# Kernel optimization log

Hardware: AMD Instinct MI355X
Metric: run time of the kernel (lower is better)

The kernel has to match this reference:

```python
import jax, jax.numpy as jnp
import numpy as np

B, S, E = 2, 2048, 1024
H, D = 16, 64


def setup_inputs() -> dict:
    key = jax.random.key(0)
    ks = jax.random.split(key, 9)
    s_in = 1.0 / np.sqrt(E)
    s_out = 1.0 / np.sqrt(H * D)
    return {
        "x": jax.random.normal(ks[0], (B, S, E), dtype=jnp.float32),
        "W_q": jax.random.uniform(ks[1], (H, E, D), jnp.float32, -s_in, s_in),
        "b_q": jax.random.uniform(ks[2], (H, D), jnp.float32, -s_in, s_in),
        "W_k": jax.random.uniform(ks[3], (H, E, D), jnp.float32, -s_in, s_in),
        "b_k": jax.random.uniform(ks[4], (H, D), jnp.float32, -s_in, s_in),
        "W_v": jax.random.uniform(ks[5], (H, E, D), jnp.float32, -s_in, s_in),
        "b_v": jax.random.uniform(ks[6], (H, D), jnp.float32, -s_in, s_in),
        "W_o": jax.random.uniform(ks[7], (H * D, E), jnp.float32, -s_out, s_out),
        "b_o": jax.random.uniform(ks[8], (E,), jnp.float32, -s_out, s_out),
    }


def reference(x, W_q, b_q, W_k, b_k, W_v, b_v, W_o, b_o):
    # batched per-head projections: [B,S,E] x [H,E,D] -> [B,H,S,D]
    q = jnp.einsum("bse,hed->bhsd", x, W_q) + b_q[None, :, None, :]
    k = jnp.einsum("bse,hed->bhsd", x, W_k) + b_k[None, :, None, :]
    v = jnp.einsum("bse,hed->bhsd", x, W_v) + b_v[None, :, None, :]
    scale = 1.0 / jnp.sqrt(jnp.asarray(D, dtype=x.dtype))
    score = jnp.einsum("bhsd,bhtd->bhst", q, k) * scale  # [B,H,S,S]
    causal = jnp.tril(jnp.ones((S, S), dtype=bool))
    score = jnp.where(causal[None, None], score, -jnp.inf)
    w = jax.nn.softmax(score, axis=-1)
    o = jnp.einsum("bhst,bhtd->bhsd", w, v)  # [B,H,S,D]
    # concat heads along last dim (head-major order matches torch.cat)
    o = o.transpose(0, 2, 1, 3).reshape(B, S, H * D)
    # dropout is identity in eval mode
    return o @ W_o + b_o
```

## Files before the change

kernel.cpp:

```cpp
#include <hip/hip_runtime.h>


typedef __attribute__((ext_vector_type(8)))  __bf16 bf16x8;
typedef __attribute__((ext_vector_type(4)))  __bf16 bf16x4;
typedef __attribute__((ext_vector_type(2)))  __bf16 bf16x2;
typedef __attribute__((ext_vector_type(4)))  float  f32x4;
typedef __attribute__((ext_vector_type(16))) float  f32x16;
typedef __attribute__((ext_vector_type(2)))  unsigned int u32x2;
typedef __attribute__((ext_vector_type(4)))  unsigned int u32x4;

#define LOG2E 1.4426950408889634f
#define SM_SC (0.125f * LOG2E)

static __device__ __forceinline__ void gl2lds16(const void* g, void* l) {
    __builtin_amdgcn_global_load_lds(
        (__attribute__((address_space(1))) void*)(void*)g,
        (__attribute__((address_space(3))) void*)l, 16, 0, 0);
}

static __device__ __forceinline__ unsigned pku(float a, float b) {
    bf16x2 t = { (__bf16)a, (__bf16)b };
    return __builtin_bit_cast(unsigned, t);
}

__global__ void prep_x_kern(const float* __restrict__ x, __bf16* __restrict__ xb) {
    int i = (blockIdx.x * 256 + threadIdx.x) * 4;
    f32x4 v = *(const f32x4*)(x + i);
    bf16x4 o = { (__bf16)v[0], (__bf16)v[1], (__bf16)v[2], (__bf16)v[3] };
    *(bf16x4*)(xb + i) = o;
}

__global__ void __launch_bounds__(256)
prep_wqkv_kern(const float* __restrict__ Wq, const float* __restrict__ Wk,
               const float* __restrict__ Wv, const float* __restrict__ bq,
               const float* __restrict__ bk, const float* __restrict__ bv,
               __bf16* __restrict__ wt, float* __restrict__ bias) {
    __shared__ float T[64][65];
    const int t = threadIdx.x;
    const int blk = blockIdx.x;
    const int kt = blk & 15, ph = blk >> 4;
    const int h = ph & 15, p = ph >> 4;
    const float* W  = (p == 0) ? Wq : (p == 1) ? Wk : Wv;
    const float* bb = (p == 0) ? bq : (p == 1) ? bk : bv;
    #pragma unroll
    for (int i = 0; i < 4; ++i) {
        int flat = i * 1024 + t * 4;
        int kr = flat >> 6, d4 = flat & 63;
        f32x4 v = *(const f32x4*)(W + (h << 16) + ((kt * 64 + kr) << 6) + d4);
        T[kr][d4] = v[0]; T[kr][d4 + 1] = v[1]; T[kr][d4 + 2] = v[2]; T[kr][d4 + 3] = v[3];
    }
    __syncthreads();
    const int d = t >> 2, kq = (t & 3) << 4;
    bf16x8 o0, o1;
    #pragma unroll
    for (int j = 0; j < 8; ++j) o0[j] = (__bf16)T[kq + j][d];
    #pragma unroll
    for (int j = 0; j < 8; ++j) o1[j] = (__bf16)T[kq + 8 + j][d];
    __bf16* dst = wt + (((size_t)(p * 1024 + h * 64 + d)) << 10) + kt * 64 + kq;
    *(bf16x8*)dst = o0;
    *(bf16x8*)(dst + 8) = o1;
    if (kt == 0 && t < 64) bias[p * 1024 + h * 64 + t] = bb[h * 64 + t];
}

__global__ void __launch_bounds__(256)
prep_wo_kern(const float* __restrict__ Wo, __bf16* __restrict__ wt) {
    __shared__ float T[64][65];
    const int t = threadIdx.x;
    const int nt = blockIdx.x & 15, ktile = blockIdx.x >> 4;
    #pragma unroll
    for (int i = 0; i < 4; ++i) {
        int flat = i * 1024 + t * 4;
        int kr = flat >> 6, n4 = flat & 63;
        f32x4 v = *(const f32x4*)(Wo + ((size_t)(ktile * 64 + kr) << 10) + nt * 64 + n4);
        T[kr][n4] = v[0]; T[kr][n4 + 1] = v[1]; T[kr][n4 + 2] = v[2]; T[kr][n4 + 3] = v[3];
    }
    __syncthreads();
    const int n = t >> 2, kq = (t & 3) << 4;
    bf16x8 o0, o1;
    #pragma unroll
    for (int j = 0; j < 8; ++j) o0[j] = (__bf16)T[kq + j][n];
    #pragma unroll
    for (int j = 0; j < 8; ++j) o1[j] = (__bf16)T[kq + 8 + j][n];
    __bf16* dst = wt + (((size_t)(nt * 64 + n)) << 10) + ktile * 64 + kq;
    *(bf16x8*)dst = o0;
    *(bf16x8*)(dst + 8) = o1;
}

template <int EPI>
__global__ void __launch_bounds__(256, 2)
gemm_bt(const __bf16* __restrict__ A, const __bf16* __restrict__ Bt,
        const float* __restrict__ bias,
        __bf16* __restrict__ outq, __bf16* __restrict__ outk, __bf16* __restrict__ outv,
        float* __restrict__ outf)
{
    __shared__ __align__(16) __bf16 As[128 * 64];
    __shared__ __align__(16) __bf16 Bs[128 * 64];
    const int tid = threadIdx.x;
    const int wid = tid >> 6, lane = tid & 63;
    const int r = lane & 15, g = lane >> 4;
    const int m0 = blockIdx.y << 7, n0 = blockIdx.x << 7;
    const int wr = wid >> 1, wc = wid & 1;
    f32x4 acc[4][4] = {};
    for (int k0 = 0; k0 < 1024; k0 += 64) {
        #pragma unroll
        for (int c = 0; c < 4; ++c) {
            int cq = (c * 4 + wid) * 64 + lane;
            int row = cq >> 3, ci = cq & 7;
            gl2lds16(A  + (((size_t)(m0 + row)) << 10) + k0 + ci * 8, As + (c * 4 + wid) * 512);
            gl2lds16(Bt + (((size_t)(n0 + row)) << 10) + k0 + ci * 8, Bs + (c * 4 + wid) * 512);
        }
        __syncthreads();
        bf16x8 af[2][4], bfr[2][4];
        #pragma unroll
        for (int kh = 0; kh < 2; ++kh)
            #pragma unroll
            for (int i = 0; i < 4; ++i) {
                af[kh][i]  = *(const bf16x8*)&As[(wr * 64 + i * 16 + r) * 64 + kh * 32 + g * 8];
                bfr[kh][i] = *(const bf16x8*)&Bs[(wc * 64 + i * 16 + r) * 64 + kh * 32 + g * 8];
            }
        #pragma unroll
        for (int kh = 0; kh < 2; ++kh)
            #pragma unroll
            for (int mi = 0; mi < 4; ++mi)
                #pragma unroll
                for (int ni = 0; ni < 4; ++ni)
                    acc[mi][ni] = __builtin_amdgcn_mfma_f32_16x16x32_bf16(
                        af[kh][mi], bfr[kh][ni], acc[mi][ni], 0, 0, 0);
        __syncthreads();
    }
    if (EPI == 0) {
        #pragma unroll
        for (int ni = 0; ni < 4; ++ni) {
            int n = n0 + wc * 64 + ni * 16 + r;
            float bv = bias[n];
            int p = n >> 10, rem = n & 1023, h = rem >> 6, d = rem & 63;
            #pragma unroll
            for (int mi = 0; mi < 4; ++mi) {
                int mb = m0 + wr * 64 + mi * 16 + g * 4;
                int b = mb >> 11, s = mb & 2047;
                f32x4 v = acc[mi][ni];
                if (p < 2) {
                    __bf16* dst = (p == 0) ? outq : outk;
                    size_t base = (((size_t)(b * 16 + h)) * 2048 + s) * 64 + d;
                    #pragma unroll
                    for (int j = 0; j < 4; ++j)
                        dst[base + (size_t)j * 64] = (__bf16)(v[j] + bv);
                } else {
                    bf16x4 pk = { (__bf16)(v[0] + bv), (__bf16)(v[1] + bv),
                                  (__bf16)(v[2] + bv), (__bf16)(v[3] + bv) };
                    *(bf16x4*)&outv[(((size_t)(b * 16 + h)) * 64 + d) * 2048 + s] = pk;
                }
            }
        }
    } else {
        #pragma unroll
        for (int ni = 0; ni < 4; ++ni) {
            int n = n0 + wc * 64 + ni * 16 + r;
            float bv = bias[n];
            #pragma unroll
            for (int mi = 0; mi < 4; ++mi) {
                int mb = m0 + wr * 64 + mi * 16 + g * 4;
                f32x4 v = acc[mi][ni];
                #pragma unroll
                for (int j = 0; j < 4; ++j)
                    outf[((size_t)(mb + j) << 10) + n] = v[j] + bv;
            }
        }
    }
}

__global__ void __launch_bounds__(256, 3)
attn_kern(const __bf16* __restrict__ q, const __bf16* __restrict__ k,
          const __bf16* __restrict__ vT, __bf16* __restrict__ pO0,
          __bf16* __restrict__ pO1, float* __restrict__ ml)
{
    __shared__ __align__(16) __bf16 Ks [2][64][72];
    __shared__ __align__(16) __bf16 VsT[2][64][72];
    const int tid = threadIdx.x, lane = tid & 63, w = tid >> 6;
    const int r31 = lane & 31, hi = lane >> 5;
    const int x = blockIdx.x & 7, kvh = blockIdx.x >> 3;
    const int bh = blockIdx.y, b = bh >> 4, h = bh & 15;
    const __bf16* qh  = q  + ((size_t)bh << 17);
    const __bf16* khp = k  + ((size_t)bh << 17);
    const __bf16* vhp = vT + ((size_t)bh << 17);
    __bf16* pO = kvh ? pO1 : pO0;
    const int srow = tid >> 3, sci = tid & 7;

    bf16x8 onesf;
    #pragma unroll
    for (int j = 0; j < 8; ++j) onesf[j] = (__bf16)1.0f;

    for (int seg = 0; seg < 2; ++seg) {
        const int xq = (seg == 0) ? (15 - x) : x;
        const int qb0 = xq << 7;
        const int wrow0 = qb0 + w * 32;
        const int mg = wrow0 + r31;
        const int tbeg = kvh * (xq + 1), tend = tbeg + (xq + 1);

        bf16x8 qf[4];
        #pragma unroll
        for (int kk = 0; kk < 4; ++kk)
            qf[kk] = *(const bf16x8*)&qh[(size_t)mg * 64 + kk * 16 + hi * 8];

        f32x16 oacc[2] = {};
        f32x16 lacc = {};
        float mrun = -3.0e38f;

        #pragma unroll
        for (int it = 0; it < 2; ++it) {
            int row = srow + it * 32;
            *(bf16x8*)&Ks [0][row][sci * 8] = *(const bf16x8*)&khp[(size_t)(tbeg * 64 + row) * 64 + sci * 8];
            *(bf16x8*)&VsT[0][row][sci * 8] = *(const bf16x8*)&vhp[(size_t)row * 2048 + tbeg * 64 + sci * 8];
        }
        __syncthreads();

        for (int t = tbeg; t < tend; ++t) {
            const int cur = (t - tbeg) & 1, nxt = cur ^ 1;
            const int n0 = t << 6;
            const bool pre = (t + 1 < tend);
            bf16x8 nk[2], nv[2];
            if (pre) {
                int n1 = n0 + 64;
                #pragma unroll
                for (int it = 0; it < 2; ++it) {
                    int row = srow + it * 32;
                    nk[it] = *(const bf16x8*)&khp[(size_t)(n1 + row) * 64 + sci * 8];
                    nv[it] = *(const bf16x8*)&vhp[(size_t)row * 2048 + n1 + sci * 8];
                }
            }
            if (n0 <= wrow0 + 31) {
                f32x16 sacc[2] = {};
                #pragma unroll
                for (int kk = 0; kk < 4; ++kk) {
                    bf16x8 kf0 = *(const bf16x8*)&Ks[cur][r31]     [kk * 16 + hi * 8];
                    bf16x8 kf1 = *(const bf16x8*)&Ks[cur][32 + r31][kk * 16 + hi * 8];
                    sacc[0] = __builtin_amdgcn_mfma_f32_32x32x16_bf16(kf0, qf[kk], sacc[0], 0, 0, 0);
                    sacc[1] = __builtin_amdgcn_mfma_f32_32x32x16_bf16(kf1, qf[kk], sacc[1], 0, 0, 0);
                }
                if (n0 + 63 > wrow0) {
                    #pragma unroll
                    for (int nf = 0; nf < 2; ++nf)
                        #pragma unroll
                        for (int i = 0; i < 16; ++i) {
                            int n = n0 + nf * 32 + (i & 3) + 8 * (i >> 2) + 4 * hi;
                            if (n > mg) sacc[nf][i] = -3.0e38f;
                        }
                }
                float mx[16];
                #pragma unroll
                for (int i = 0; i < 16; ++i) mx[i] = fmaxf(sacc[0][i], sacc[1][i]);
                #pragma unroll
                for (int s = 8; s > 0; s >>= 1)
                    #pragma unroll
                    for (int i = 0; i < 8; ++i)
                        if (i < s) mx[i] = fmaxf(mx[i], mx[i + s]);
                float pmh = mx[0];
                if (!__all((pmh - mrun) * SM_SC <= 8.0f)) {
                    float pm = fmaxf(pmh, __shfl_xor(pmh, 32));
                    float mnew = fmaxf(mrun, pm);
                    float fac = exp2f((mrun - mnew) * SM_SC);
                    lacc[0] *= fac;
                    #pragma unroll
                    for (int df = 0; df < 2; ++df)
                        #pragma unroll
                        for (int i = 0; i < 16; ++i) oacc[df][i] *= fac;
                    mrun = mnew;
                }
                #pragma unroll
                for (int nf = 0; nf < 2; ++nf)
                    #pragma unroll
                    for (int i = 0; i < 16; ++i)
                        sacc[nf][i] = exp2f((sacc[nf][i] - mrun) * SM_SC);
                #pragma unroll
                for (int nf = 0; nf < 2; ++nf) {
                    unsigned pk[8];
                    #pragma unroll
                    for (int j = 0; j < 8; ++j)
                        pk[j] = pku(sacc[nf][2 * j], sacc[nf][2 * j + 1]);
#if __has_builtin(__builtin_amdgcn_permlane32_swap)
                    u32x2 s02 = __builtin_amdgcn_permlane32_swap(pk[0], pk[2], false, false);
                    u32x2 s13 = __builtin_amdgcn_permlane32_swap(pk[1], pk[3], false, false);
                    u32x2 s46 = __builtin_amdgcn_permlane32_swap(pk[4], pk[6], false, false);
                    u32x2 s57 = __builtin_amdgcn_permlane32_swap(pk[5], pk[7], false, false);
                    u32x4 fw0 = { s02[0], s13[0], s02[1], s13[1] };
                    u32x4 fw1 = { s46[0], s57[0], s46[1], s57[1] };
#else
                    unsigned rxa = __shfl_xor(hi ? pk[0] : pk[2], 32);
                    unsigned rxb = __shfl_xor(hi ? pk[1] : pk[3], 32);
                    unsigned rxc = __shfl_xor(hi ? pk[4] : pk[6], 32);
                    unsigned rxd = __shfl_xor(hi ? pk[5] : pk[7], 32);
                    u32x4 fw0 = { hi ? rxa : pk[0], hi ? rxb : pk[1],
                                  hi ? pk[2] : rxa, hi ? pk[3] : rxb };
                    u32x4 fw1 = { hi ? rxc : pk[4], hi ? rxd : pk[5],
                                  hi ? pk[6] : rxc, hi ? pk[7] : rxd };
#endif
                    bf16x8 pf0 = __builtin_bit_cast(bf16x8, fw0);
                    bf16x8 pf1 = __builtin_bit_cast(bf16x8, fw1);
                    #pragma unroll
                    for (int kl = 0; kl < 2; ++kl) {
                        const bf16x8 pf = kl ? pf1 : pf0;
                        const int kk = nf * 2 + kl;
                        bf16x8 af0 = *(const bf16x8*)&VsT[cur][r31]     [kk * 16 + hi * 8];
                        bf16x8 af1 = *(const bf16x8*)&VsT[cur][32 + r31][kk * 16 + hi * 8];
                        oacc[0] = __builtin_amdgcn_mfma_f32_32x32x16_bf16(af0, pf, oacc[0], 0, 0, 0);
                        oacc[1] = __builtin_amdgcn_mfma_f32_32x32x16_bf16(af1, pf, oacc[1], 0, 0, 0);
                        lacc    = __builtin_amdgcn_mfma_f32_32x32x16_bf16(onesf, pf, lacc, 0, 0, 0);
                    }
                }
            }
            if (pre) {
                #pragma unroll
                for (int it = 0; it < 2; ++it) {
                    int row = srow + it * 32;
                    *(bf16x8*)&Ks [nxt][row][sci * 8] = nk[it];
                    *(bf16x8*)&VsT[nxt][row][sci * 8] = nv[it];
                }
            }
            __syncthreads();
        }
        float lrun = lacc[0];
        float inv = (lrun > 0.f) ? 1.0f / lrun : 0.f;
        #pragma unroll
        for (int df = 0; df < 2; ++df)
            #pragma unroll
            for (int td = 0; td < 8; ++td) {
                bf16x2 pr = { (__bf16)(oacc[df][2 * td] * inv),
                              (__bf16)(oacc[df][2 * td + 1] * inv) };
                int d = df * 32 + 8 * (td >> 1) + 4 * hi + 2 * (td & 1);
                *(bf16x2*)&pO[((size_t)(b * 2048 + mg) << 10) + h * 64 + d] = pr;
            }
        if (hi == 0) {
            size_t mi = (((size_t)kvh * 32 + bh) * 2048 + mg) * 2;
            ml[mi] = mrun;
            ml[mi + 1] = lrun;
        }
    }
}

__global__ void merge_kern(const __bf16* __restrict__ pO0, const float* __restrict__ ml,
                           __bf16* __restrict__ ob)
{
    int i = blockIdx.x * 256 + threadIdx.x;
    int m = i >> 7, rem = i & 127, h = rem >> 3, d8 = (rem & 7) * 8;
    int bh = (m >> 11) * 16 + h, sr = m & 2047;
    size_t i0 = ((size_t)bh * 2048 + sr) * 2;
    float m0 = ml[i0], l0 = ml[i0 + 1];
    float m1 = ml[131072 + i0], l1 = ml[131072 + i0 + 1];
    float mx = fmaxf(m0, m1);
    float c0 = exp2f((m0 - mx) * SM_SC) * l0;
    float c1 = exp2f((m1 - mx) * SM_SC) * l1;
    float inv = 1.0f / (c0 + c1);
    float w0 = c0 * inv, w1 = c1 * inv;
    size_t off = (size_t)m * 1024 + h * 64 + d8;
    bf16x8 a = *(const bf16x8*)(pO0 + off);
    bf16x8 c = *(const bf16x8*)(ob + off);
    bf16x8 r;
    #pragma unroll
    for (int j = 0; j < 8; ++j) r[j] = (__bf16)(w0 * (float)a[j] + w1 * (float)c[j]);
    *(bf16x8*)(ob + off) = r;
}

extern "C" void kernel_launch(void* const* d_in, const int* in_sizes, int n_in,
                              void* d_out, int out_size, void* d_ws, size_t ws_size,
                              hipStream_t stream) {
    const float* x  = (const float*)d_in[0];
    const float* Wq = (const float*)d_in[1];
    const float* bq = (const float*)d_in[2];
    const float* Wk = (const float*)d_in[3];
    const float* bk = (const float*)d_in[4];
    const float* Wv = (const float*)d_in[5];
    const float* bv = (const float*)d_in[6];
    const float* Wo = (const float*)d_in[7];
    const float* bo = (const float*)d_in[8];
    float* out = (float*)d_out;
    char* ws = (char*)d_ws;
    __bf16* xb    = (__bf16*)(ws + 0);
    __bf16* wtqkv = (__bf16*)(ws + 8388608);
    __bf16* wot   = (__bf16*)(ws + 14680064);
    float*  biasq = (float*) (ws + 16777216);
    __bf16* qb    = (__bf16*)(ws + 16793600);
    __bf16* kb    = (__bf16*)(ws + 25182208);
    __bf16* vtb   = (__bf16*)(ws + 33570816);
    __bf16* ob    = (__bf16*)(ws + 41959424);
    __bf16* pO0   = xb;
    float*  mlbuf = (float*)(ws + 8388608);

    prep_x_kern<<<4096, 256, 0, stream>>>(x, xb);
    prep_wqkv_kern<<<768, 256, 0, stream>>>(Wq, Wk, Wv, bq, bk, bv, wtqkv, biasq);
    prep_wo_kern<<<256, 256, 0, stream>>>(Wo, wot);
    gemm_bt<0><<<dim3(24, 32), 256, 0, stream>>>(xb, wtqkv, biasq, qb, kb, vtb, nullptr);
    attn_kern<<<dim3(16, 32), 256, 0, stream>>>(qb, kb, vtb, pO0, ob, mlbuf);
    merge_kern<<<4096, 256, 0, stream>>>(pO0, mlbuf, ob);
    gemm_bt<1><<<dim3(8, 32), 256, 0, stream>>>(ob, wot, bo, nullptr, nullptr, nullptr, out);
}
```

Measured before the change: 132.0 us.

## Split attention KV tiles across two wave groups with in-block softmax merge

The attention block grows to 512 threads, split into two groups of four waves that process alternate KV tiles of the same query rows. The two partial results are then merged through shared memory with the usual max/sum rescaling. The row-sum is now computed with a VALU reduction instead of an extra MFMA against a ones vector, and the double buffer is replaced by one tile per group. The aim is more in-flight waves per query block and less MFMA work. In exchange it adds a shared-memory merge, an extra barrier and more register pressure under the new launch bounds.

```diff
diff --git a/kernel.cpp b/kernel.cpp
--- a/kernel.cpp
+++ b/kernel.cpp
@@ -169,14 +169,20 @@
     }
 }
 
-__global__ void __launch_bounds__(256, 3)
+__global__ void __launch_bounds__(512, 4)
 attn_kern(const __bf16* __restrict__ q, const __bf16* __restrict__ k,
           const __bf16* __restrict__ vT, __bf16* __restrict__ pO0,
           __bf16* __restrict__ pO1, float* __restrict__ ml)
 {
-    __shared__ __align__(16) __bf16 Ks [2][64][72];
-    __shared__ __align__(16) __bf16 VsT[2][64][72];
+    __shared__ __align__(16) char smem_raw[36864];
+    __shared__ float ML[4][64][2];
+    typedef __bf16 TileT[64][72];
+    TileT* Ks  = (TileT*)smem_raw;
+    TileT* VsT = (TileT*)(smem_raw + 18432);
+    float* OM  = (float*)smem_raw;
+
     const int tid = threadIdx.x, lane = tid & 63, w = tid >> 6;
+    const int grp = w >> 2, wl = w & 3;
     const int r31 = lane & 31, hi = lane >> 5;
     const int x = blockIdx.x & 7, kvh = blockIdx.x >> 3;
     const int bh = blockIdx.y, b = bh >> 4, h = bh & 15;
@@ -184,18 +190,17 @@
     const __bf16* khp = k  + ((size_t)bh << 17);
     const __bf16* vhp = vT + ((size_t)bh << 17);
     __bf16* pO = kvh ? pO1 : pO0;
-    const int srow = tid >> 3, sci = tid & 7;
-
-    bf16x8 onesf;
-    #pragma unroll
-    for (int j = 0; j < 8; ++j) onesf[j] = (__bf16)1.0f;
+    const int tb = tid >> 8, inner = tid & 255;
+    const int srow = inner >> 3, sci = inner & 7;
 
     for (int seg = 0; seg < 2; ++seg) {
-        const int xq = (seg == 0) ? (15 - x) : x;
-        const int qb0 = xq << 7;
-        const int wrow0 = qb0 + w * 32;
+        const int j = (seg == 0) ? (15 - x) : x;
+        const int qb0 = j << 7;
+        const int wrow0 = qb0 + wl * 32;
         const int mg = wrow0 + r31;
-        const int tbeg = kvh * (xq + 1), tend = tbeg + (xq + 1);
+        const int c = j + 1;
+        const int tbeg = kvh * c;
+        const int S = (c + 1) >> 1;
 
         bf16x8 qf[4];
         #pragma unroll
@@ -203,37 +208,40 @@
             qf[kk] = *(const bf16x8*)&qh[(size_t)mg * 64 + kk * 16 + hi * 8];
 
         f32x16 oacc[2] = {};
-        f32x16 lacc = {};
-        float mrun = -3.0e38f;
-
-        #pragma unroll
-        for (int it = 0; it < 2; ++it) {
-            int row = srow + it * 32;
-            *(bf16x8*)&Ks [0][row][sci * 8] = *(const bf16x8*)&khp[(size_t)(tbeg * 64 + row) * 64 + sci * 8];
-            *(bf16x8*)&VsT[0][row][sci * 8] = *(const bf16x8*)&vhp[(size_t)row * 2048 + tbeg * 64 + sci * 8];
-        }
+        float mrun = -3.0e38f, lrun = 0.f;
+
         __syncthreads();
-
-        for (int t = tbeg; t < tend; ++t) {
-            const int cur = (t - tbeg) & 1, nxt = cur ^ 1;
-            const int n0 = t << 6;
-            const bool pre = (t + 1 < tend);
+        {
+            int tg = min(tbeg + tb, 31);
+            #pragma unroll
+            for (int it = 0; it < 2; ++it) {
+                int row = srow + it * 32;
+                *(bf16x8*)&Ks [tb][row][sci * 8] = *(const bf16x8*)&khp[(size_t)(tg * 64 + row) * 64 + sci * 8];
+                *(bf16x8*)&VsT[tb][row][sci * 8] = *(const bf16x8*)&vhp[(size_t)row * 2048 + tg * 64 + sci * 8];
+            }
+        }
+        __syncthreads();
+
+        for (int s = 0; s < S; ++s) {
+            const bool pre = (s + 1 < S);
             bf16x8 nk[2], nv[2];
             if (pre) {
-                int n1 = n0 + 64;
+                int tg = min(tbeg + 2 * (s + 1) + tb, 31);
                 #pragma unroll
                 for (int it = 0; it < 2; ++it) {
                     int row = srow + it * 32;
-                    nk[it] = *(const bf16x8*)&khp[(size_t)(n1 + row) * 64 + sci * 8];
-                    nv[it] = *(const bf16x8*)&vhp[(size_t)row * 2048 + n1 + sci * 8];
-                }
-            }
-            if (n0 <= wrow0 + 31) {
+                    nk[it] = *(const bf16x8*)&khp[(size_t)(tg * 64 + row) * 64 + sci * 8];
+                    nv[it] = *(const bf16x8*)&vhp[(size_t)row * 2048 + tg * 64 + sci * 8];
+                }
+            }
+            const int t = tbeg + 2 * s + grp;
+            const int n0 = t << 6;
+            if ((2 * s + grp < c) && (n0 <= wrow0 + 31)) {
                 f32x16 sacc[2] = {};
                 #pragma unroll
                 for (int kk = 0; kk < 4; ++kk) {
-                    bf16x8 kf0 = *(const bf16x8*)&Ks[cur][r31]     [kk * 16 + hi * 8];
-                    bf16x8 kf1 = *(const bf16x8*)&Ks[cur][32 + r31][kk * 16 + hi * 8];
+                    bf16x8 kf0 = *(const bf16x8*)&Ks[grp][r31]     [kk * 16 + hi * 8];
+                    bf16x8 kf1 = *(const bf16x8*)&Ks[grp][32 + r31][kk * 16 + hi * 8];
                     sacc[0] = __builtin_amdgcn_mfma_f32_32x32x16_bf16(kf0, qf[kk], sacc[0], 0, 0, 0);
                     sacc[1] = __builtin_amdgcn_mfma_f32_32x32x16_bf16(kf1, qf[kk], sacc[1], 0, 0, 0);
                 }
@@ -250,16 +258,16 @@
                 #pragma unroll
                 for (int i = 0; i < 16; ++i) mx[i] = fmaxf(sacc[0][i], sacc[1][i]);
                 #pragma unroll
-                for (int s = 8; s > 0; s >>= 1)
+                for (int st = 8; st > 0; st >>= 1)
                     #pragma unroll
                     for (int i = 0; i < 8; ++i)
-                        if (i < s) mx[i] = fmaxf(mx[i], mx[i + s]);
+                        if (i < st) mx[i] = fmaxf(mx[i], mx[i + st]);
                 float pmh = mx[0];
                 if (!__all((pmh - mrun) * SM_SC <= 8.0f)) {
                     float pm = fmaxf(pmh, __shfl_xor(pmh, 32));
                     float mnew = fmaxf(mrun, pm);
                     float fac = exp2f((mrun - mnew) * SM_SC);
-                    lacc[0] *= fac;
+                    lrun *= fac;
                     #pragma unroll
                     for (int df = 0; df < 2; ++df)
                         #pragma unroll
@@ -271,12 +279,23 @@
                     #pragma unroll
                     for (int i = 0; i < 16; ++i)
                         sacc[nf][i] = exp2f((sacc[nf][i] - mrun) * SM_SC);
+                {
+                    float smv[16];
+                    #pragma unroll
+                    for (int i = 0; i < 16; ++i) smv[i] = sacc[0][i] + sacc[1][i];
+                    #pragma unroll
+                    for (int st = 8; st > 0; st >>= 1)
+                        #pragma unroll
+                        for (int i = 0; i < 8; ++i)
+                            if (i < st) smv[i] += smv[i + st];
+                    lrun += smv[0] + __shfl_xor(smv[0], 32);
+                }
                 #pragma unroll
                 for (int nf = 0; nf < 2; ++nf) {
                     unsigned pk[8];
                     #pragma unroll
-                    for (int j = 0; j < 8; ++j)
-                        pk[j] = pku(sacc[nf][2 * j], sacc[nf][2 * j + 1]);
+                    for (int jj = 0; jj < 8; ++jj)
+                        pk[jj] = pku(sacc[nf][2 * jj], sacc[nf][2 * jj + 1]);
 #if __has_builtin(__builtin_amdgcn_permlane32_swap)
                     u32x2 s02 = __builtin_amdgcn_permlane32_swap(pk[0], pk[2], false, false);
                     u32x2 s13 = __builtin_amdgcn_permlane32_swap(pk[1], pk[3], false, false);
@@ -300,11 +319,10 @@
                     for (int kl = 0; kl < 2; ++kl) {
                         const bf16x8 pf = kl ? pf1 : pf0;
                         const int kk = nf * 2 + kl;
-                        bf16x8 af0 = *(const bf16x8*)&VsT[cur][r31]     [kk * 16 + hi * 8];
-                        bf16x8 af1 = *(const bf16x8*)&VsT[cur][32 + r31][kk * 16 + hi * 8];
+                        bf16x8 af0 = *(const bf16x8*)&VsT[grp][r31]     [kk * 16 + hi * 8];
+                        bf16x8 af1 = *(const bf16x8*)&VsT[grp][32 + r31][kk * 16 + hi * 8];
                         oacc[0] = __builtin_amdgcn_mfma_f32_32x32x16_bf16(af0, pf, oacc[0], 0, 0, 0);
                         oacc[1] = __builtin_amdgcn_mfma_f32_32x32x16_bf16(af1, pf, oacc[1], 0, 0, 0);
-                        lacc    = __builtin_amdgcn_mfma_f32_32x32x16_bf16(onesf, pf, lacc, 0, 0, 0);
                     }
                 }
             }
@@ -312,27 +330,45 @@
                 #pragma unroll
                 for (int it = 0; it < 2; ++it) {
                     int row = srow + it * 32;
-                    *(bf16x8*)&Ks [nxt][row][sci * 8] = nk[it];
-                    *(bf16x8*)&VsT[nxt][row][sci * 8] = nv[it];
+                    *(bf16x8*)&Ks [tb][row][sci * 8] = nk[it];
+                    *(bf16x8*)&VsT[tb][row][sci * 8] = nv[it];
                 }
             }
             __syncthreads();
         }
-        float lrun = lacc[0];
-        float inv = (lrun > 0.f) ? 1.0f / lrun : 0.f;
-        #pragma unroll
-        for (int df = 0; df < 2; ++df)
-            #pragma unroll
-            for (int td = 0; td < 8; ++td) {
-                bf16x2 pr = { (__bf16)(oacc[df][2 * td] * inv),
-                              (__bf16)(oacc[df][2 * td + 1] * inv) };
-                int d = df * 32 + 8 * (td >> 1) + 4 * hi + 2 * (td & 1);
-                *(bf16x2*)&pO[((size_t)(b * 2048 + mg) << 10) + h * 64 + d] = pr;
-            }
-        if (hi == 0) {
-            size_t mi = (((size_t)kvh * 32 + bh) * 2048 + mg) * 2;
-            ml[mi] = mrun;
-            ml[mi + 1] = lrun;
+        if (grp == 0) {
+            float* dst = OM + (wl * 64 + lane) * 33;
+            #pragma unroll
+            for (int df = 0; df < 2; ++df)
+                #pragma unroll
+                for (int i = 0; i < 16; ++i) dst[df * 16 + i] = oacc[df][i];
+            ML[wl][lane][0] = mrun;
+            ML[wl][lane][1] = lrun;
+        }
+        __syncthreads();
+        if (grp == 1) {
+            const float* src = OM + (wl * 64 + lane) * 33;
+            float mA = ML[wl][lane][0], lA = ML[wl][lane][1];
+            float ms = fmaxf(mA, mrun);
+            float wA = exp2f((mA - ms) * SM_SC);
+            float wB = exp2f((mrun - ms) * SM_SC);
+            float lC = wA * lA + wB * lrun;
+            float inv = (lC > 0.f) ? 1.0f / lC : 0.f;
+            #pragma unroll
+            for (int df = 0; df < 2; ++df)
+                #pragma unroll
+                for (int td = 0; td < 8; ++td) {
+                    float a0 = wA * src[df * 16 + 2 * td]     + wB * oacc[df][2 * td];
+                    float a1 = wA * src[df * 16 + 2 * td + 1] + wB * oacc[df][2 * td + 1];
+                    bf16x2 pr = { (__bf16)(a0 * inv), (__bf16)(a1 * inv) };
+                    int d = df * 32 + 8 * (td >> 1) + 4 * hi + 2 * (td & 1);
+                    *(bf16x2*)&pO[((size_t)(b * 2048 + mg) << 10) + h * 64 + d] = pr;
+                }
+            if (hi == 0) {
+                size_t mi = (((size_t)kvh * 32 + bh) * 2048 + mg) * 2;
+                ml[mi] = ms;
+                ml[mi + 1] = lC;
+            }
         }
     }
 }
@@ -389,7 +425,7 @@
     prep_wqkv_kern<<<768, 256, 0, stream>>>(Wq, Wk, Wv, bq, bk, bv, wtqkv, biasq);
     prep_wo_kern<<<256, 256, 0, stream>>>(Wo, wot);
     gemm_bt<0><<<dim3(24, 32), 256, 0, stream>>>(xb, wtqkv, biasq, qb, kb, vtb, nullptr);
-    attn_kern<<<dim3(16, 32), 256, 0, stream>>>(qb, kb, vtb, pO0, ob, mlbuf);
+    attn_kern<<<dim3(16, 32), 512, 0, stream>>>(qb, kb, vtb, pO0, ob, mlbuf);
     merge_kern<<<4096, 256, 0, stream>>>(pO0, mlbuf, ob);
     gemm_bt<1><<<dim3(8, 32), 256, 0, stream>>>(ob, wot, bo, nullptr, nullptr, nullptr, out);
 }
```

Result: slower. 171.0 us (+29.6%).
